# Kernel optimization log

Measured on AMD Instinct MI355X. Metric: run time of the kernel, lower is better.

## Reference

```python
import jax, jax.numpy as jnp
import numpy as np

N_NODES = 100000


def sage_conv(x, src, dst, Wl, Wr, b):
    # mean-aggregate neighbor (source) features onto destinations
    msg = x[src]                                              # [E, F]
    agg = jax.ops.segment_sum(msg, dst, num_segments=N_NODES)  # [N, F]
    deg = jax.ops.segment_sum(jnp.ones(dst.shape, x.dtype), dst, num_segments=N_NODES)
    agg = agg / jnp.maximum(deg, 1.0)[:, None]
    # PyG SAGEConv: lin_l(aggr) + lin_r(x); bias only on lin_l
    return agg @ Wl.T + x @ Wr.T + b


def setup_inputs() -> dict:
    key = jax.random.key(0)
    ks = jax.random.split(key, 12)
    d, h, c = 128, 128, 6
    s = 1.0 / np.sqrt(d)
    return {
        "x": jax.random.normal(ks[0], (N_NODES, d), jnp.float32),
        "edge_index": jax.random.randint(ks[1], (2, 3200000), 0, N_NODES, jnp.int64),
        "Wl1": jax.random.normal(ks[2], (h, d), jnp.float32) * s,
        "Wr1": jax.random.normal(ks[3], (h, d), jnp.float32) * s,
        "b1": jax.random.normal(ks[4], (h,), jnp.float32) * s,
        "Wl2": jax.random.normal(ks[5], (h, h), jnp.float32) * s,
        "Wr2": jax.random.normal(ks[6], (h, h), jnp.float32) * s,
        "b2": jax.random.normal(ks[7], (h,), jnp.float32) * s,
        "Wl3": jax.random.normal(ks[8], (c, h), jnp.float32) * s,
        "Wr3": jax.random.normal(ks[9], (c, h), jnp.float32) * s,
        "b3": jax.random.normal(ks[10], (c,), jnp.float32) * s,
    }


def reference(x, edge_index, Wl1, Wr1, b1, Wl2, Wr2, b2, Wl3, Wr3, b3):
    src, dst = edge_index[0], edge_index[1]
    h = jax.nn.relu(sage_conv(x, src, dst, Wl1, Wr1, b1))  # dropout = identity (eval)
    h = jax.nn.relu(sage_conv(h, src, dst, Wl2, Wr2, b2))
    return sage_conv(h, src, dst, Wl3, Wr3, b3)  # [N, 6]
```

## Files before the change

kernel.cpp:

```cpp
#include <hip/hip_runtime.h>
#include <hip/hip_bf16.h>

#define N_NODES 100000
#define G_PART 16
#define B_PART 96
#define NPG_PAD 6272
#define A_BLOCKS 1024

__global__ __launch_bounds__(256) void partition_edges(
    const int* __restrict__ src, const int* __restrict__ dst, int E,
    int* __restrict__ bkt, unsigned int* __restrict__ gcur, int cap, int npg) {
    __shared__ int cnt16[G_PART];
    __shared__ unsigned int base16[G_PART];
    __shared__ unsigned int cur16[G_PART];
    int tid = threadIdx.x;
    if (tid < G_PART) cnt16[tid] = 0;
    __syncthreads();
    int per = (E + A_BLOCKS - 1) / A_BLOCKS;
    int beg = blockIdx.x * per;
    int end = min(beg + per, E);
    for (int i = beg + tid; i < end; i += 256) {
        int d = dst[i];
        atomicAdd(&cnt16[d / npg], 1);
    }
    __syncthreads();
    if (tid < G_PART) {
        base16[tid] = atomicAdd(&gcur[tid], (unsigned int)cnt16[tid]);
        cur16[tid] = 0;
    }
    __syncthreads();
    for (int i = beg + tid; i < end; i += 256) {
        int d = dst[i];
        int s = src[i];
        int g = d / npg;
        unsigned int p = base16[g] + atomicAdd(&cur16[g], 1u);
        bkt[(size_t)g * cap + p] = ((d - g * npg) << 17) | s;
    }
}

__global__ __launch_bounds__(256) void count_hist(const int* __restrict__ bkt,
                                                  const unsigned int* __restrict__ gcur,
                                                  int cap, unsigned short* __restrict__ partial,
                                                  int npg, int N) {
    __shared__ int hist[NPG_PAD];
    int g = blockIdx.x & (G_PART - 1);
    int b = blockIdx.x / G_PART;
    int tid = threadIdx.x;
    for (int i = tid; i < npg; i += 256) hist[i] = 0;
    __syncthreads();
    int len = (int)gcur[g];
    int per = (len + B_PART - 1) / B_PART;
    int ibeg = b * per;
    int iend = min(ibeg + per, len);
    const int* bp = bkt + (size_t)g * cap;
    for (int i = ibeg + tid; i < iend; i += 256) {
        int v = __builtin_nontemporal_load(bp + i);
        atomicAdd(&hist[v >> 17], 1);
    }
    __syncthreads();
    size_t base = (size_t)(g * B_PART + b) * npg;
    for (int j = tid; j < npg; j += 256) partial[base + j] = (unsigned short)hist[j];
}

__global__ __launch_bounds__(256) void scan_partials(unsigned short* __restrict__ partial,
                                                     int* __restrict__ cnt,
                                                     int npg, int N) {
    int n = blockIdx.x * 256 + threadIdx.x;
    if (n >= N) return;
    int g = n / npg;
    int i = n - g * npg;
    size_t base = (size_t)g * B_PART * npg + i;
    int run = 0;
#pragma unroll 4
    for (int b = 0; b < B_PART; ++b) {
        size_t idx = base + (size_t)b * npg;
        int t = partial[idx];
        partial[idx] = (unsigned short)run;
        run += t;
    }
    cnt[n] = run;
}

__global__ __launch_bounds__(256) void fill_hist(const int* __restrict__ bkt,
                                                 const unsigned int* __restrict__ gcur,
                                                 int cap,
                                                 const unsigned short* __restrict__ partial,
                                                 const int* __restrict__ row_off,
                                                 int* __restrict__ csr_src,
                                                 int npg, int N) {
    __shared__ int cur[NPG_PAD];
    int g = blockIdx.x & (G_PART - 1);
    int b = blockIdx.x / G_PART;
    int lo = g * npg;
    int tid = threadIdx.x;
    size_t pbase = (size_t)(g * B_PART + b) * npg;
    for (int i = tid; i < npg && lo + i < N; i += 256)
        cur[i] = row_off[lo + i] + (int)partial[pbase + i];
    __syncthreads();
    int len = (int)gcur[g];
    int per = (len + B_PART - 1) / B_PART;
    int ibeg = b * per;
    int iend = min(ibeg + per, len);
    const int* bp = bkt + (size_t)g * cap;
    for (int i = ibeg + tid; i < iend; i += 256) {
        int v = __builtin_nontemporal_load(bp + i);
        int p = atomicAdd(&cur[v >> 17], 1);
        csr_src[p] = v & 0x1FFFF;
    }
}

#define SCHUNK 1024

__global__ __launch_bounds__(256) void scan_blocks(const int* __restrict__ cnt,
                                                   int* __restrict__ row_off,
                                                   int* __restrict__ block_sums, int n) {
    __shared__ int ts[256];
    int tid = threadIdx.x;
    int base = blockIdx.x * SCHUNK + tid * 4;
    int v[4];
    int s = 0;
#pragma unroll
    for (int j = 0; j < 4; ++j) {
        int i = base + j;
        v[j] = (i < n) ? cnt[i] : 0;
        s += v[j];
    }
    ts[tid] = s;
    __syncthreads();
    for (int off = 1; off < 256; off <<= 1) {
        int t = 0;
        if (tid >= off) t = ts[tid - off];
        __syncthreads();
        if (tid >= off) ts[tid] += t;
        __syncthreads();
    }
    int run = (tid > 0) ? ts[tid - 1] : 0;
    if (tid == 255) block_sums[blockIdx.x] = ts[255];
#pragma unroll
    for (int j = 0; j < 4; ++j) {
        int i = base + j;
        if (i < n) row_off[i] = run;
        run += v[j];
    }
}

__global__ __launch_bounds__(256) void scan_sums(int* __restrict__ block_sums, int nb,
                                                 int* __restrict__ row_off, int n) {
    __shared__ int ts[256];
    int tid = threadIdx.x;
    int v = (tid < nb) ? block_sums[tid] : 0;
    ts[tid] = v;
    __syncthreads();
    for (int off = 1; off < 256; off <<= 1) {
        int t = 0;
        if (tid >= off) t = ts[tid - off];
        __syncthreads();
        if (tid >= off) ts[tid] += t;
        __syncthreads();
    }
    if (tid < nb) block_sums[tid] = (tid > 0) ? ts[tid - 1] : 0;
    if (tid == 255) row_off[n] = ts[255];
}

__global__ __launch_bounds__(256) void scan_add(int* __restrict__ row_off,
                                                const int* __restrict__ block_sums, int n) {
    int tid = threadIdx.x;
    int off = block_sums[blockIdx.x];
    int base = blockIdx.x * SCHUNK + tid * 4;
#pragma unroll
    for (int j = 0; j < 4; ++j) {
        int i = base + j;
        if (i < n) row_off[i] += off;
    }
}

__global__ __launch_bounds__(256) void pack_bf16(const float* __restrict__ in,
                                                 uint2* __restrict__ out, int n4) {
    int i = blockIdx.x * 256 + threadIdx.x;
    if (i >= n4) return;
    float4 v = *(const float4*)&in[(size_t)i * 4];
    __hip_bfloat162 p0 = __float22bfloat162_rn(make_float2(v.x, v.y));
    __hip_bfloat162 p1 = __float22bfloat162_rn(make_float2(v.z, v.w));
    uint2 o;
    o.x = *(const uint*)&p0;
    o.y = *(const uint*)&p1;
    out[i] = o;
}

static __device__ inline unsigned short f2bf(float v) {
    __hip_bfloat16 b = __float2bfloat16(v);
    return *(const unsigned short*)&b;
}

__global__ __launch_bounds__(256) void pack_weights(
    const float* __restrict__ Wl1, const float* __restrict__ Wr1,
    const float* __restrict__ Wl2, const float* __restrict__ Wr2,
    const float* __restrict__ Wl3, const float* __restrict__ Wr3,
    unsigned short* __restrict__ Wc1, unsigned short* __restrict__ Wc2,
    unsigned short* __restrict__ W3c) {
    int idx = blockIdx.x * 256 + threadIdx.x;
    if (idx < 32768) {
        int n = idx >> 8, k = idx & 255;
        Wc1[idx] = f2bf((k < 128) ? Wl1[n * 128 + k] : Wr1[n * 128 + (k - 128)]);
    } else if (idx < 65536) {
        int t = idx - 32768;
        int n = t >> 8, k = t & 255;
        Wc2[t] = f2bf((k < 128) ? Wl2[n * 128 + k] : Wr2[n * 128 + (k - 128)]);
    } else if (idx < 65536 + 2048) {
        int t = idx - 65536;
        int n = t >> 7, k = t & 127;
        float v = (n < 6) ? Wl3[n * 128 + k] : ((n < 12) ? Wr3[(n - 6) * 128 + k] : 0.f);
        W3c[t] = f2bf(v);
    }
}

typedef __attribute__((ext_vector_type(8))) short bfrag8;
typedef __attribute__((ext_vector_type(4))) float f32x4;

static __device__ inline float2 unpack2(uint v) {
    float2 r;
    r.x = __uint_as_float(v << 16);
    r.y = __uint_as_float(v & 0xffff0000u);
    return r;
}

__global__ __launch_bounds__(256) void agg_gemm(
    const uint* __restrict__ featb,
    const unsigned short* __restrict__ Aself,
    const int* __restrict__ row_off,
    const int* __restrict__ csr,
    const unsigned short* __restrict__ Wc,
    const float* __restrict__ bias,
    unsigned short* __restrict__ outb,
    int do_lin3,
    const unsigned short* __restrict__ W3c,
    const float* __restrict__ b3,
    unsigned short* __restrict__ zg,
    float* __restrict__ zs,
    int M, int relu) {
    __shared__ unsigned short aggT[16][136];
    __shared__ unsigned short h2T[16][136];
    int tid = threadIdx.x;
    int wave = tid >> 6;
    int lane = tid & 63;
    int tile = blockIdx.x * 16;
    int mrow = lane & 15;
    int quad = lane >> 4;
    int row = tile + mrow;
    int rc = (row < M) ? row : 0;

    bfrag8 aself[4];
    const unsigned short* arow1 = Aself + (size_t)rc * 128;
#pragma unroll
    for (int ks = 0; ks < 4; ++ks)
        aself[ks] = *(const bfrag8*)(arow1 + ks * 32 + quad * 8);
    int t0 = wave * 2, t1 = wave * 2 + 1;
    float bc0 = bias[t0 * 16 + mrow];
    float bc1 = bias[t1 * 16 + mrow];

    for (int sub = 0; sub < 4; ++sub) {
        int node = tile + wave * 4 + sub;
        float sx = 0.f, sy = 0.f;
        float inv = 0.f;
        if (node < M) {
            int beg = row_off[node], end = row_off[node + 1];
            int i = beg;
            for (; i + 4 <= end; i += 4) {
                int s0 = csr[i], s1 = csr[i + 1], s2 = csr[i + 2], s3 = csr[i + 3];
                uint v0 = featb[(size_t)s0 * 64 + lane];
                uint v1 = featb[(size_t)s1 * 64 + lane];
                uint v2 = featb[(size_t)s2 * 64 + lane];
                uint v3 = featb[(size_t)s3 * 64 + lane];
                float2 f0 = unpack2(v0), f1 = unpack2(v1);
                float2 f2 = unpack2(v2), f3 = unpack2(v3);
                sx += f0.x + f1.x + f2.x + f3.x;
                sy += f0.y + f1.y + f2.y + f3.y;
            }
            for (; i < end; ++i) {
                uint v = featb[(size_t)csr[i] * 64 + lane];
                float2 f = unpack2(v);
                sx += f.x;
                sy += f.y;
            }
            inv = (end > beg) ? 1.0f / (float)(end - beg) : 0.0f;
        }
        __hip_bfloat162 p = __float22bfloat162_rn(make_float2(sx * inv, sy * inv));
        *(uint*)&aggT[wave * 4 + sub][lane * 2] = *(const uint*)&p;
    }
    __syncthreads();

    f32x4 acc0 = (f32x4){0.f, 0.f, 0.f, 0.f};
    f32x4 acc1 = (f32x4){0.f, 0.f, 0.f, 0.f};
#pragma unroll
    for (int ks = 0; ks < 8; ++ks) {
        bfrag8 af;
        if (ks < 4) af = *(const bfrag8*)&aggT[mrow][ks * 32 + quad * 8];
        else af = aself[ks - 4];
        bfrag8 bf0 = *(const bfrag8*)(Wc + (size_t)(t0 * 16 + mrow) * 256 + ks * 32 + quad * 8);
        bfrag8 bf1 = *(const bfrag8*)(Wc + (size_t)(t1 * 16 + mrow) * 256 + ks * 32 + quad * 8);
        acc0 = __builtin_amdgcn_mfma_f32_16x16x32_bf16(af, bf0, acc0, 0, 0, 0);
        acc1 = __builtin_amdgcn_mfma_f32_16x16x32_bf16(af, bf1, acc1, 0, 0, 0);
    }
#pragma unroll
    for (int tt = 0; tt < 2; ++tt) {
        f32x4 a = tt ? acc1 : acc0;
        int col = (wave * 2 + tt) * 16 + mrow;
        float bc = tt ? bc1 : bc0;
#pragma unroll
        for (int r = 0; r < 4; ++r) {
            float v = a[r] + bc;
            if (relu) v = fmaxf(v, 0.f);
            h2T[quad * 4 + r][col] = f2bf(v);
        }
    }
    __syncthreads();
    if (outb) {
        int r = tid >> 4;
        int c8 = (tid & 15) * 8;
        int orow = tile + r;
        if (orow < M)
            *(uint4*)&outb[(size_t)orow * 128 + c8] = *(const uint4*)&h2T[r][c8];
    }
    if (do_lin3 && wave == 0) {
        f32x4 acc = (f32x4){0.f, 0.f, 0.f, 0.f};
#pragma unroll
        for (int ks = 0; ks < 4; ++ks) {
            bfrag8 af = *(const bfrag8*)&h2T[mrow][ks * 32 + quad * 8];
            bfrag8 bf = *(const bfrag8*)(W3c + (size_t)mrow * 128 + ks * 32 + quad * 8);
            acc = __builtin_amdgcn_mfma_f32_16x16x32_bf16(af, bf, acc, 0, 0, 0);
        }
        int col = mrow;
#pragma unroll
        for (int r = 0; r < 4; ++r) {
            int orow = tile + quad * 4 + r;
            if (orow < M) {
                float v = acc[r];
                if (col < 6) {
                    zg[(size_t)orow * 8 + col] = f2bf(v);
                } else if (col < 12) {
                    zs[(size_t)orow * 6 + (col - 6)] = v + b3[col - 6];
                }
            }
        }
    }
}

__global__ void out_kernel(const unsigned short* __restrict__ zg,
                           const float* __restrict__ zs,
                           const int* __restrict__ row_off,
                           const int* __restrict__ csr,
                           float* __restrict__ out, int M) {
    int idx = blockIdx.x * blockDim.x + threadIdx.x;
    int node = idx >> 3;
    int j = idx & 7;
    if (node >= M || j >= 6) return;
    int beg = row_off[node], end = row_off[node + 1];
    float acc = 0.f;
    int i = beg;
    for (; i + 4 <= end; i += 4) {
        int s0 = csr[i], s1 = csr[i + 1], s2 = csr[i + 2], s3 = csr[i + 3];
        uint z0 = zg[(size_t)s0 * 8 + j];
        uint z1 = zg[(size_t)s1 * 8 + j];
        uint z2 = zg[(size_t)s2 * 8 + j];
        uint z3 = zg[(size_t)s3 * 8 + j];
        acc += __uint_as_float(z0 << 16) + __uint_as_float(z1 << 16) +
               __uint_as_float(z2 << 16) + __uint_as_float(z3 << 16);
    }
    for (; i < end; ++i) {
        uint z = zg[(size_t)csr[i] * 8 + j];
        acc += __uint_as_float(z << 16);
    }
    float inv = (end > beg) ? 1.0f / (float)(end - beg) : 0.0f;
    out[(size_t)node * 6 + j] = acc * inv + zs[(size_t)node * 6 + j];
}

static inline size_t align_up(size_t x, size_t a) { return (x + a - 1) & ~(a - 1); }

extern "C" void kernel_launch(void* const* d_in, const int* in_sizes, int n_in,
                              void* d_out, int out_size, void* d_ws, size_t ws_size,
                              hipStream_t stream) {
    const float* x = (const float*)d_in[0];
    const int* ei = (const int*)d_in[1];
    const float* Wl1 = (const float*)d_in[2];
    const float* Wr1 = (const float*)d_in[3];
    const float* b1 = (const float*)d_in[4];
    const float* Wl2 = (const float*)d_in[5];
    const float* Wr2 = (const float*)d_in[6];
    const float* b2 = (const float*)d_in[7];
    const float* Wl3 = (const float*)d_in[8];
    const float* Wr3 = (const float*)d_in[9];
    const float* b3 = (const float*)d_in[10];

    const int N = in_sizes[0] / 128;
    const int E = in_sizes[1] / 2;
    const int* src = ei;
    const int* dst = ei + E;

    char* ws = (char*)d_ws;
    size_t off = 0;
    int* cnt = (int*)(ws + off);        off = align_up(off + (size_t)N * 4, 512);
    int* row_off = (int*)(ws + off);    off = align_up(off + (size_t)(N + 1) * 4, 512);
    int* block_sums = (int*)(ws + off); off = align_up(off + 512 * 4, 512);
    unsigned int* gcur = (unsigned int*)(ws + off); off = align_up(off + 64 * 4, 512);
    unsigned short* Wc1 = (unsigned short*)(ws + off); off = align_up(off + 128 * 256 * 2, 512);
    unsigned short* Wc2 = (unsigned short*)(ws + off); off = align_up(off + 128 * 256 * 2, 512);
    unsigned short* W3c = (unsigned short*)(ws + off); off = align_up(off + 16 * 128 * 2, 512);
    int* csr_src = (int*)(ws + off);    off = align_up(off + (size_t)E * 4, 512);
    float* slotA = (float*)(ws + off);  off = align_up(off + (size_t)N * 128 * 4, 512);
    float* slotB = (float*)(ws + off);  off = align_up(off + (size_t)N * 128 * 4, 512);
    uint2* h1b = (uint2*)(ws + off);    off = align_up(off + (size_t)N * 128 * 2, 512);
    unsigned short* partial = (unsigned short*)slotA;
    const int cap = 210000;
    int* bkt = (int*)slotB;
    uint2* xb = (uint2*)slotA;
    unsigned short* zg = (unsigned short*)slotB;
    float* zs = (float*)((char*)slotB + align_up((size_t)N * 8 * 2, 512));
    (void)ws_size;

    const int npg = (N + G_PART - 1) / G_PART;
    const int build_grid = G_PART * B_PART;

    hipMemsetAsync(gcur, 0, G_PART * 4, stream);
    partition_edges<<<A_BLOCKS, 256, 0, stream>>>(src, dst, E, bkt, gcur, cap, npg);
    count_hist<<<build_grid, 256, 0, stream>>>(bkt, gcur, cap, partial, npg, N);
    scan_partials<<<(N + 255) / 256, 256, 0, stream>>>(partial, cnt, npg, N);

    const int nscan = (N + SCHUNK - 1) / SCHUNK;
    scan_blocks<<<nscan, 256, 0, stream>>>(cnt, row_off, block_sums, N);
    scan_sums<<<1, 256, 0, stream>>>(block_sums, nscan, row_off, N);
    scan_add<<<nscan, 256, 0, stream>>>(row_off, block_sums, N);

    fill_hist<<<build_grid, 256, 0, stream>>>(bkt, gcur, cap, partial, row_off,
                                              csr_src, npg, N);

    const int n4 = N * 32;
    pack_bf16<<<(n4 + 255) / 256, 256, 0, stream>>>(x, xb, n4);
    pack_weights<<<(65536 + 2048 + 255) / 256, 256, 0, stream>>>(
        Wl1, Wr1, Wl2, Wr2, Wl3, Wr3, Wc1, Wc2, W3c);

    int fusedGrid = (N + 15) / 16;

    agg_gemm<<<fusedGrid, 256, 0, stream>>>(
        (const uint*)xb, (const unsigned short*)xb, row_off, csr_src, Wc1, b1,
        (unsigned short*)h1b, 0, nullptr, nullptr, nullptr, nullptr, N, 1);
    agg_gemm<<<fusedGrid, 256, 0, stream>>>(
        (const uint*)h1b, (const unsigned short*)h1b, row_off, csr_src, Wc2, b2,
        nullptr, 1, W3c, b3, zg, zs, N, 1);
    out_kernel<<<(N * 8 + 255) / 256, 256, 0, stream>>>(zg, zs, row_off, csr_src,
                                                        (float*)d_out, N);
}
```

Before: 577.3 us.

## Bin CSR edges by source range and sweep source ranges across node blocks

The CSR build now sorts each destination's edges into 8 source-range sub-bins, using 128 destination partitions with finer partial histograms. The aggregation kernel handles 64 nodes per block and loops over source ranges in the outer loop, so concurrent gathers touch a narrower slice of the feature table and get better cache locality. The cost is an 8x larger offset array and scan, more per-node offset loads, 32 accumulator registers per thread with an occupancy hint, and per-tile syncs inside the GEMM loop.

```diff
diff --git a/kernel.cpp b/kernel.cpp
--- a/kernel.cpp
+++ b/kernel.cpp
@@ -2,51 +2,57 @@
 #include <hip/hip_bf16.h>
 
 #define N_NODES 100000
-#define G_PART 16
-#define B_PART 96
-#define NPG_PAD 6272
+#define G_PART 128
+#define NPG 782
+#define NR 8
+#define RNG 12500
+#define BINS (NPG * NR)
+#define BINS_PAD 6272
+#define B_PART 12
 #define A_BLOCKS 1024
+#define NBINS (N_NODES * NR)
+#define NPB 64
 
 __global__ __launch_bounds__(256) void partition_edges(
     const int* __restrict__ src, const int* __restrict__ dst, int E,
-    int* __restrict__ bkt, unsigned int* __restrict__ gcur, int cap, int npg) {
-    __shared__ int cnt16[G_PART];
-    __shared__ unsigned int base16[G_PART];
-    __shared__ unsigned int cur16[G_PART];
-    int tid = threadIdx.x;
-    if (tid < G_PART) cnt16[tid] = 0;
+    int* __restrict__ bkt, unsigned int* __restrict__ gcur, int cap) {
+    __shared__ int cnt[G_PART];
+    __shared__ unsigned int base[G_PART];
+    __shared__ unsigned int cur[G_PART];
+    int tid = threadIdx.x;
+    if (tid < G_PART) cnt[tid] = 0;
     __syncthreads();
     int per = (E + A_BLOCKS - 1) / A_BLOCKS;
     int beg = blockIdx.x * per;
     int end = min(beg + per, E);
     for (int i = beg + tid; i < end; i += 256) {
         int d = dst[i];
-        atomicAdd(&cnt16[d / npg], 1);
+        atomicAdd(&cnt[d / NPG], 1);
     }
     __syncthreads();
     if (tid < G_PART) {
-        base16[tid] = atomicAdd(&gcur[tid], (unsigned int)cnt16[tid]);
-        cur16[tid] = 0;
+        base[tid] = atomicAdd(&gcur[tid], (unsigned int)cnt[tid]);
+        cur[tid] = 0;
     }
     __syncthreads();
     for (int i = beg + tid; i < end; i += 256) {
         int d = dst[i];
         int s = src[i];
-        int g = d / npg;
-        unsigned int p = base16[g] + atomicAdd(&cur16[g], 1u);
-        bkt[(size_t)g * cap + p] = ((d - g * npg) << 17) | s;
+        int g = d / NPG;
+        unsigned int p = base[g] + atomicAdd(&cur[g], 1u);
+        bkt[(size_t)g * cap + p] = ((d - g * NPG) << 17) | s;
     }
 }
 
 __global__ __launch_bounds__(256) void count_hist(const int* __restrict__ bkt,
                                                   const unsigned int* __restrict__ gcur,
-                                                  int cap, unsigned short* __restrict__ partial,
-                                                  int npg, int N) {
-    __shared__ int hist[NPG_PAD];
+                                                  int cap,
+                                                  unsigned short* __restrict__ partial) {
+    __shared__ int hist[BINS_PAD];
     int g = blockIdx.x & (G_PART - 1);
     int b = blockIdx.x / G_PART;
     int tid = threadIdx.x;
-    for (int i = tid; i < npg; i += 256) hist[i] = 0;
+    for (int i = tid; i < BINS; i += 256) hist[i] = 0;
     __syncthreads();
     int len = (int)gcur[g];
     int per = (len + B_PART - 1) / B_PART;
@@ -55,47 +61,113 @@
     const int* bp = bkt + (size_t)g * cap;
     for (int i = ibeg + tid; i < iend; i += 256) {
         int v = __builtin_nontemporal_load(bp + i);
-        atomicAdd(&hist[v >> 17], 1);
-    }
-    __syncthreads();
-    size_t base = (size_t)(g * B_PART + b) * npg;
-    for (int j = tid; j < npg; j += 256) partial[base + j] = (unsigned short)hist[j];
+        int bin = (v >> 17) * NR + (v & 0x1FFFF) / RNG;
+        atomicAdd(&hist[bin], 1);
+    }
+    __syncthreads();
+    size_t basep = (size_t)(g * B_PART + b) * BINS;
+    for (int j = tid; j < BINS; j += 256) partial[basep + j] = (unsigned short)hist[j];
 }
 
 __global__ __launch_bounds__(256) void scan_partials(unsigned short* __restrict__ partial,
-                                                     int* __restrict__ cnt,
-                                                     int npg, int N) {
-    int n = blockIdx.x * 256 + threadIdx.x;
-    if (n >= N) return;
-    int g = n / npg;
-    int i = n - g * npg;
-    size_t base = (size_t)g * B_PART * npg + i;
+                                                     int* __restrict__ cnt) {
+    int B = blockIdx.x * 256 + threadIdx.x;
+    if (B >= NBINS) return;
+    int g = B / BINS;
+    int i = B - g * BINS;
+    size_t basep = (size_t)g * B_PART * BINS + i;
     int run = 0;
 #pragma unroll 4
     for (int b = 0; b < B_PART; ++b) {
-        size_t idx = base + (size_t)b * npg;
+        size_t idx = basep + (size_t)b * BINS;
         int t = partial[idx];
         partial[idx] = (unsigned short)run;
         run += t;
     }
-    cnt[n] = run;
+    cnt[B] = run;
+}
+
+#define SCHUNK 4096
+
+__global__ __launch_bounds__(256) void scan_blocks(const int* __restrict__ cnt,
+                                                   int* __restrict__ boff,
+                                                   int* __restrict__ block_sums, int n) {
+    __shared__ int ts[256];
+    int tid = threadIdx.x;
+    int base = blockIdx.x * SCHUNK + tid * 16;
+    int v[16];
+    int s = 0;
+#pragma unroll
+    for (int j = 0; j < 16; ++j) {
+        int i = base + j;
+        v[j] = (i < n) ? cnt[i] : 0;
+        s += v[j];
+    }
+    ts[tid] = s;
+    __syncthreads();
+    for (int off = 1; off < 256; off <<= 1) {
+        int t = 0;
+        if (tid >= off) t = ts[tid - off];
+        __syncthreads();
+        if (tid >= off) ts[tid] += t;
+        __syncthreads();
+    }
+    int run = (tid > 0) ? ts[tid - 1] : 0;
+    if (tid == 255) block_sums[blockIdx.x] = ts[255];
+#pragma unroll
+    for (int j = 0; j < 16; ++j) {
+        int i = base + j;
+        if (i < n) boff[i] = run;
+        run += v[j];
+    }
+}
+
+__global__ __launch_bounds__(256) void scan_sums(int* __restrict__ block_sums, int nb,
+                                                 int* __restrict__ boff, int n) {
+    __shared__ int ts[256];
+    int tid = threadIdx.x;
+    int v = (tid < nb) ? block_sums[tid] : 0;
+    ts[tid] = v;
+    __syncthreads();
+    for (int off = 1; off < 256; off <<= 1) {
+        int t = 0;
+        if (tid >= off) t = ts[tid - off];
+        __syncthreads();
+        if (tid >= off) ts[tid] += t;
+        __syncthreads();
+    }
+    if (tid < nb) block_sums[tid] = (tid > 0) ? ts[tid - 1] : 0;
+    if (tid == 255) boff[n] = ts[255];
+}
+
+__global__ __launch_bounds__(256) void scan_add(int* __restrict__ boff,
+                                                const int* __restrict__ block_sums, int n) {
+    int tid = threadIdx.x;
+    int off = block_sums[blockIdx.x];
+    int base = blockIdx.x * SCHUNK + tid * 16;
+#pragma unroll
+    for (int j = 0; j < 16; ++j) {
+        int i = base + j;
+        if (i < n) boff[i] += off;
+    }
 }
 
 __global__ __launch_bounds__(256) void fill_hist(const int* __restrict__ bkt,
                                                  const unsigned int* __restrict__ gcur,
                                                  int cap,
                                                  const unsigned short* __restrict__ partial,
-                                                 const int* __restrict__ row_off,
-                                                 int* __restrict__ csr_src,
-                                                 int npg, int N) {
-    __shared__ int cur[NPG_PAD];
+                                                 const int* __restrict__ boff,
+                                                 int* __restrict__ csr_src) {
+    __shared__ int cur[BINS_PAD];
     int g = blockIdx.x & (G_PART - 1);
     int b = blockIdx.x / G_PART;
-    int lo = g * npg;
-    int tid = threadIdx.x;
-    size_t pbase = (size_t)(g * B_PART + b) * npg;
-    for (int i = tid; i < npg && lo + i < N; i += 256)
-        cur[i] = row_off[lo + i] + (int)partial[pbase + i];
+    int tid = threadIdx.x;
+    size_t pbase = (size_t)(g * B_PART + b) * BINS;
+    int gb = g * BINS;
+    for (int i = tid; i < BINS; i += 256) {
+        int node = g * NPG + (i >> 3);
+        if (node < N_NODES) cur[i] = boff[gb + i] + (int)partial[pbase + i];
+    }
     __syncthreads();
     int len = (int)gcur[g];
     int per = (len + B_PART - 1) / B_PART;
@@ -104,73 +176,9 @@
     const int* bp = bkt + (size_t)g * cap;
     for (int i = ibeg + tid; i < iend; i += 256) {
         int v = __builtin_nontemporal_load(bp + i);
-        int p = atomicAdd(&cur[v >> 17], 1);
+        int bin = (v >> 17) * NR + (v & 0x1FFFF) / RNG;
+        int p = atomicAdd(&cur[bin], 1);
         csr_src[p] = v & 0x1FFFF;
-    }
-}
-
-#define SCHUNK 1024
-
-__global__ __launch_bounds__(256) void scan_blocks(const int* __restrict__ cnt,
-                                                   int* __restrict__ row_off,
-                                                   int* __restrict__ block_sums, int n) {
-    __shared__ int ts[256];
-    int tid = threadIdx.x;
-    int base = blockIdx.x * SCHUNK + tid * 4;
-    int v[4];
-    int s = 0;
-#pragma unroll
-    for (int j = 0; j < 4; ++j) {
-        int i = base + j;
-        v[j] = (i < n) ? cnt[i] : 0;
-        s += v[j];
-    }
-    ts[tid] = s;
-    __syncthreads();
-    for (int off = 1; off < 256; off <<= 1) {
-        int t = 0;
-        if (tid >= off) t = ts[tid - off];
-        __syncthreads();
-        if (tid >= off) ts[tid] += t;
-        __syncthreads();
-    }
-    int run = (tid > 0) ? ts[tid - 1] : 0;
-    if (tid == 255) block_sums[blockIdx.x] = ts[255];
-#pragma unroll
-    for (int j = 0; j < 4; ++j) {
-        int i = base + j;
-        if (i < n) row_off[i] = run;
-        run += v[j];
-    }
-}
-
-__global__ __launch_bounds__(256) void scan_sums(int* __restrict__ block_sums, int nb,
-                                                 int* __restrict__ row_off, int n) {
-    __shared__ int ts[256];
-    int tid = threadIdx.x;
-    int v = (tid < nb) ? block_sums[tid] : 0;
-    ts[tid] = v;
-    __syncthreads();
-    for (int off = 1; off < 256; off <<= 1) {
-        int t = 0;
-        if (tid >= off) t = ts[tid - off];
-        __syncthreads();
-        if (tid >= off) ts[tid] += t;
-        __syncthreads();
-    }
-    if (tid < nb) block_sums[tid] = (tid > 0) ? ts[tid - 1] : 0;
-    if (tid == 255) row_off[n] = ts[255];
-}
-
-__global__ __launch_bounds__(256) void scan_add(int* __restrict__ row_off,
-                                                const int* __restrict__ block_sums, int n) {
-    int tid = threadIdx.x;
-    int off = block_sums[blockIdx.x];
-    int base = blockIdx.x * SCHUNK + tid * 4;
-#pragma unroll
-    for (int j = 0; j < 4; ++j) {
-        int i = base + j;
-        if (i < n) row_off[i] += off;
     }
 }
 
@@ -224,10 +232,10 @@
     return r;
 }
 
-__global__ __launch_bounds__(256) void agg_gemm(
+__global__ __launch_bounds__(256, 6) void agg_gemm(
     const uint* __restrict__ featb,
     const unsigned short* __restrict__ Aself,
-    const int* __restrict__ row_off,
+    const int* __restrict__ boff,
     const int* __restrict__ csr,
     const unsigned short* __restrict__ Wc,
     const float* __restrict__ bias,
@@ -243,118 +251,141 @@
     int tid = threadIdx.x;
     int wave = tid >> 6;
     int lane = tid & 63;
-    int tile = blockIdx.x * 16;
     int mrow = lane & 15;
     int quad = lane >> 4;
-    int row = tile + mrow;
-    int rc = (row < M) ? row : 0;
-
-    bfrag8 aself[4];
-    const unsigned short* arow1 = Aself + (size_t)rc * 128;
-#pragma unroll
-    for (int ks = 0; ks < 4; ++ks)
-        aself[ks] = *(const bfrag8*)(arow1 + ks * 32 + quad * 8);
+    int base = blockIdx.x * NPB;
+
+    float accx[16], accy[16];
+#pragma unroll
+    for (int k = 0; k < 16; ++k) { accx[k] = 0.f; accy[k] = 0.f; }
+
+    for (int r = 0; r < NR; ++r) {
+#pragma unroll
+        for (int k = 0; k < 16; ++k) {
+            int node = base + (k >> 2) * 16 + wave * 4 + (k & 3);
+            if (node < M) {
+                const int* bo = boff + node * NR + r;
+                int beg = bo[0], end = bo[1];
+                float sx = accx[k], sy = accy[k];
+                int i = beg;
+                for (; i + 4 <= end; i += 4) {
+                    int s0 = csr[i], s1 = csr[i + 1], s2 = csr[i + 2], s3 = csr[i + 3];
+                    uint v0 = featb[(size_t)s0 * 64 + lane];
+                    uint v1 = featb[(size_t)s1 * 64 + lane];
+                    uint v2 = featb[(size_t)s2 * 64 + lane];
+                    uint v3 = featb[(size_t)s3 * 64 + lane];
+                    float2 f0 = unpack2(v0), f1 = unpack2(v1);
+                    float2 f2 = unpack2(v2), f3 = unpack2(v3);
+                    sx += f0.x + f1.x + f2.x + f3.x;
+                    sy += f0.y + f1.y + f2.y + f3.y;
+                }
+                for (; i < end; ++i) {
+                    uint v = featb[(size_t)csr[i] * 64 + lane];
+                    float2 f = unpack2(v);
+                    sx += f.x;
+                    sy += f.y;
+                }
+                accx[k] = sx;
+                accy[k] = sy;
+            }
+        }
+    }
+
     int t0 = wave * 2, t1 = wave * 2 + 1;
     float bc0 = bias[t0 * 16 + mrow];
     float bc1 = bias[t1 * 16 + mrow];
 
-    for (int sub = 0; sub < 4; ++sub) {
-        int node = tile + wave * 4 + sub;
-        float sx = 0.f, sy = 0.f;
-        float inv = 0.f;
-        if (node < M) {
-            int beg = row_off[node], end = row_off[node + 1];
-            int i = beg;
-            for (; i + 4 <= end; i += 4) {
-                int s0 = csr[i], s1 = csr[i + 1], s2 = csr[i + 2], s3 = csr[i + 3];
-                uint v0 = featb[(size_t)s0 * 64 + lane];
-                uint v1 = featb[(size_t)s1 * 64 + lane];
-                uint v2 = featb[(size_t)s2 * 64 + lane];
-                uint v3 = featb[(size_t)s3 * 64 + lane];
-                float2 f0 = unpack2(v0), f1 = unpack2(v1);
-                float2 f2 = unpack2(v2), f3 = unpack2(v3);
-                sx += f0.x + f1.x + f2.x + f3.x;
-                sy += f0.y + f1.y + f2.y + f3.y;
+#pragma unroll
+    for (int t = 0; t < 4; ++t) {
+        int tile = base + t * 16;
+#pragma unroll
+        for (int sub = 0; sub < 4; ++sub) {
+            int node = tile + wave * 4 + sub;
+            float inv = 0.f;
+            if (node < M) {
+                int b0 = boff[node * NR], e0 = boff[node * NR + NR];
+                inv = (e0 > b0) ? 1.0f / (float)(e0 - b0) : 0.f;
             }
-            for (; i < end; ++i) {
-                uint v = featb[(size_t)csr[i] * 64 + lane];
-                float2 f = unpack2(v);
-                sx += f.x;
-                sy += f.y;
+            __hip_bfloat162 p = __float22bfloat162_rn(
+                make_float2(accx[t * 4 + sub] * inv, accy[t * 4 + sub] * inv));
+            *(uint*)&aggT[wave * 4 + sub][lane * 2] = *(const uint*)&p;
+        }
+        int row = tile + mrow;
+        int rc = (row < M) ? row : 0;
+        const unsigned short* arow = Aself + (size_t)rc * 128;
+        bfrag8 aself[4];
+#pragma unroll
+        for (int ks = 0; ks < 4; ++ks)
+            aself[ks] = *(const bfrag8*)(arow + ks * 32 + quad * 8);
+        __syncthreads();
+        f32x4 acc0 = (f32x4){0.f, 0.f, 0.f, 0.f};
+        f32x4 acc1 = (f32x4){0.f, 0.f, 0.f, 0.f};
+#pragma unroll
+        for (int ks = 0; ks < 8; ++ks) {
+            bfrag8 af;
+            if (ks < 4) af = *(const bfrag8*)&aggT[mrow][ks * 32 + quad * 8];
+            else af = aself[ks - 4];
+            bfrag8 bf0 = *(const bfrag8*)(Wc + (size_t)(t0 * 16 + mrow) * 256 + ks * 32 + quad * 8);
+            bfrag8 bf1 = *(const bfrag8*)(Wc + (size_t)(t1 * 16 + mrow) * 256 + ks * 32 + quad * 8);
+            acc0 = __builtin_amdgcn_mfma_f32_16x16x32_bf16(af, bf0, acc0, 0, 0, 0);
+            acc1 = __builtin_amdgcn_mfma_f32_16x16x32_bf16(af, bf1, acc1, 0, 0, 0);
+        }
+#pragma unroll
+        for (int tt = 0; tt < 2; ++tt) {
+            f32x4 a = tt ? acc1 : acc0;
+            int col = (wave * 2 + tt) * 16 + mrow;
+            float bc = tt ? bc1 : bc0;
+#pragma unroll
+            for (int rr = 0; rr < 4; ++rr) {
+                float v = a[rr] + bc;
+                if (relu) v = fmaxf(v, 0.f);
+                h2T[quad * 4 + rr][col] = f2bf(v);
             }
-            inv = (end > beg) ? 1.0f / (float)(end - beg) : 0.0f;
-        }
-        __hip_bfloat162 p = __float22bfloat162_rn(make_float2(sx * inv, sy * inv));
-        *(uint*)&aggT[wave * 4 + sub][lane * 2] = *(const uint*)&p;
-    }
-    __syncthreads();
-
-    f32x4 acc0 = (f32x4){0.f, 0.f, 0.f, 0.f};
-    f32x4 acc1 = (f32x4){0.f, 0.f, 0.f, 0.f};
-#pragma unroll
-    for (int ks = 0; ks < 8; ++ks) {
-        bfrag8 af;
-        if (ks < 4) af = *(const bfrag8*)&aggT[mrow][ks * 32 + quad * 8];
-        else af = aself[ks - 4];
-        bfrag8 bf0 = *(const bfrag8*)(Wc + (size_t)(t0 * 16 + mrow) * 256 + ks * 32 + quad * 8);
-        bfrag8 bf1 = *(const bfrag8*)(Wc + (size_t)(t1 * 16 + mrow) * 256 + ks * 32 + quad * 8);
-        acc0 = __builtin_amdgcn_mfma_f32_16x16x32_bf16(af, bf0, acc0, 0, 0, 0);
-        acc1 = __builtin_amdgcn_mfma_f32_16x16x32_bf16(af, bf1, acc1, 0, 0, 0);
-    }
-#pragma unroll
-    for (int tt = 0; tt < 2; ++tt) {
-        f32x4 a = tt ? acc1 : acc0;
-        int col = (wave * 2 + tt) * 16 + mrow;
-        float bc = tt ? bc1 : bc0;
-#pragma unroll
-        for (int r = 0; r < 4; ++r) {
-            float v = a[r] + bc;
-            if (relu) v = fmaxf(v, 0.f);
-            h2T[quad * 4 + r][col] = f2bf(v);
-        }
-    }
-    __syncthreads();
-    if (outb) {
-        int r = tid >> 4;
-        int c8 = (tid & 15) * 8;
-        int orow = tile + r;
-        if (orow < M)
-            *(uint4*)&outb[(size_t)orow * 128 + c8] = *(const uint4*)&h2T[r][c8];
-    }
-    if (do_lin3 && wave == 0) {
-        f32x4 acc = (f32x4){0.f, 0.f, 0.f, 0.f};
-#pragma unroll
-        for (int ks = 0; ks < 4; ++ks) {
-            bfrag8 af = *(const bfrag8*)&h2T[mrow][ks * 32 + quad * 8];
-            bfrag8 bf = *(const bfrag8*)(W3c + (size_t)mrow * 128 + ks * 32 + quad * 8);
-            acc = __builtin_amdgcn_mfma_f32_16x16x32_bf16(af, bf, acc, 0, 0, 0);
-        }
-        int col = mrow;
-#pragma unroll
-        for (int r = 0; r < 4; ++r) {
-            int orow = tile + quad * 4 + r;
-            if (orow < M) {
-                float v = acc[r];
-                if (col < 6) {
-                    zg[(size_t)orow * 8 + col] = f2bf(v);
-                } else if (col < 12) {
-                    zs[(size_t)orow * 6 + (col - 6)] = v + b3[col - 6];
+        }
+        __syncthreads();
+        if (outb) {
+            int rr = tid >> 4;
+            int c8 = (tid & 15) * 8;
+            int orow = tile + rr;
+            if (orow < M)
+                *(uint4*)&outb[(size_t)orow * 128 + c8] = *(const uint4*)&h2T[rr][c8];
+        }
+        if (do_lin3 && wave == 0) {
+            f32x4 acc = (f32x4){0.f, 0.f, 0.f, 0.f};
+#pragma unroll
+            for (int ks = 0; ks < 4; ++ks) {
+                bfrag8 af = *(const bfrag8*)&h2T[mrow][ks * 32 + quad * 8];
+                bfrag8 bf = *(const bfrag8*)(W3c + (size_t)mrow * 128 + ks * 32 + quad * 8);
+                acc = __builtin_amdgcn_mfma_f32_16x16x32_bf16(af, bf, acc, 0, 0, 0);
+            }
+            int col = mrow;
+#pragma unroll
+            for (int rr = 0; rr < 4; ++rr) {
+                int orow = tile + quad * 4 + rr;
+                if (orow < M) {
+                    float v = acc[rr];
+                    if (col < 6) {
+                        zg[(size_t)orow * 8 + col] = f2bf(v);
+                    } else if (col < 12) {
+                        zs[(size_t)orow * 6 + (col - 6)] = v + b3[col - 6];
+                    }
                 }
             }
         }
+        __syncthreads();
     }
 }
 
 __global__ void out_kernel(const unsigned short* __restrict__ zg,
                            const float* __restrict__ zs,
-                           const int* __restrict__ row_off,
+                           const int* __restrict__ boff,
                            const int* __restrict__ csr,
                            float* __restrict__ out, int M) {
     int idx = blockIdx.x * blockDim.x + threadIdx.x;
     int node = idx >> 3;
     int j = idx & 7;
     if (node >= M || j >= 6) return;
-    int beg = row_off[node], end = row_off[node + 1];
+    int beg = boff[node * NR], end = boff[node * NR + NR];
     float acc = 0.f;
     int i = beg;
     for (; i + 4 <= end; i += 4) {
@@ -398,10 +429,10 @@
 
     char* ws = (char*)d_ws;
     size_t off = 0;
-    int* cnt = (int*)(ws + off);        off = align_up(off + (size_t)N * 4, 512);
-    int* row_off = (int*)(ws + off);    off = align_up(off + (size_t)(N + 1) * 4, 512);
+    int* cnt = (int*)(ws + off);        off = align_up(off + (size_t)NBINS * 4, 512);
+    int* boff = (int*)(ws + off);       off = align_up(off + (size_t)(NBINS + 1) * 4, 512);
     int* block_sums = (int*)(ws + off); off = align_up(off + 512 * 4, 512);
-    unsigned int* gcur = (unsigned int*)(ws + off); off = align_up(off + 64 * 4, 512);
+    unsigned int* gcur = (unsigned int*)(ws + off); off = align_up(off + G_PART * 4, 512);
     unsigned short* Wc1 = (unsigned short*)(ws + off); off = align_up(off + 128 * 256 * 2, 512);
     unsigned short* Wc2 = (unsigned short*)(ws + off); off = align_up(off + 128 * 256 * 2, 512);
     unsigned short* W3c = (unsigned short*)(ws + off); off = align_up(off + 16 * 128 * 2, 512);
@@ -410,42 +441,40 @@
     float* slotB = (float*)(ws + off);  off = align_up(off + (size_t)N * 128 * 4, 512);
     uint2* h1b = (uint2*)(ws + off);    off = align_up(off + (size_t)N * 128 * 2, 512);
     unsigned short* partial = (unsigned short*)slotA;
-    const int cap = 210000;
+    const int cap = 28000;
     int* bkt = (int*)slotB;
     uint2* xb = (uint2*)slotA;
     unsigned short* zg = (unsigned short*)slotB;
     float* zs = (float*)((char*)slotB + align_up((size_t)N * 8 * 2, 512));
     (void)ws_size;
 
-    const int npg = (N + G_PART - 1) / G_PART;
     const int build_grid = G_PART * B_PART;
 
     hipMemsetAsync(gcur, 0, G_PART * 4, stream);
-    partition_edges<<<A_BLOCKS, 256, 0, stream>>>(src, dst, E, bkt, gcur, cap, npg);
-    count_hist<<<build_grid, 256, 0, stream>>>(bkt, gcur, cap, partial, npg, N);
-    scan_partials<<<(N + 255) / 256, 256, 0, stream>>>(partial, cnt, npg, N);
-
-    const int nscan = (N + SCHUNK - 1) / SCHUNK;
-    scan_blocks<<<nscan, 256, 0, stream>>>(cnt, row_off, block_sums, N);
-    scan_sums<<<1, 256, 0, stream>>>(block_sums, nscan, row_off, N);
-    scan_add<<<nscan, 256, 0, stream>>>(row_off, block_sums, N);
-
-    fill_hist<<<build_grid, 256, 0, stream>>>(bkt, gcur, cap, partial, row_off,
-                                              csr_src, npg, N);
+    partition_edges<<<A_BLOCKS, 256, 0, stream>>>(src, dst, E, bkt, gcur, cap);
+    count_hist<<<build_grid, 256, 0, stream>>>(bkt, gcur, cap, partial);
+    scan_partials<<<(NBINS + 255) / 256, 256, 0, stream>>>(partial, cnt);
+
+    const int nscan = (NBINS + SCHUNK - 1) / SCHUNK;
+    scan_blocks<<<nscan, 256, 0, stream>>>(cnt, boff, block_sums, NBINS);
+    scan_sums<<<1, 256, 0, stream>>>(block_sums, nscan, boff, NBINS);
+    scan_add<<<nscan, 256, 0, stream>>>(boff, block_sums, NBINS);
+
+    fill_hist<<<build_grid, 256, 0, stream>>>(bkt, gcur, cap, partial, boff, csr_src);
 
     const int n4 = N * 32;
     pack_bf16<<<(n4 + 255) / 256, 256, 0, stream>>>(x, xb, n4);
     pack_weights<<<(65536 + 2048 + 255) / 256, 256, 0, stream>>>(
         Wl1, Wr1, Wl2, Wr2, Wl3, Wr3, Wc1, Wc2, W3c);
 
-    int fusedGrid = (N + 15) / 16;
-
-    agg_gemm<<<fusedGrid, 256, 0, stream>>>(
-        (const uint*)xb, (const unsigned short*)xb, row_off, csr_src, Wc1, b1,
+    const int aggGrid = (N + NPB - 1) / NPB;
+
+    agg_gemm<<<aggGrid, 256, 0, stream>>>(
+        (const uint*)xb, (const unsigned short*)xb, boff, csr_src, Wc1, b1,
         (unsigned short*)h1b, 0, nullptr, nullptr, nullptr, nullptr, N, 1);
-    agg_gemm<<<fusedGrid, 256, 0, stream>>>(
-        (const uint*)h1b, (const unsigned short*)h1b, row_off, csr_src, Wc2, b2,
+    agg_gemm<<<aggGrid, 256, 0, stream>>>(
+        (const uint*)h1b, (const unsigned short*)h1b, boff, csr_src, Wc2, b2,
         nullptr, 1, W3c, b3, zg, zs, N, 1);
-    out_kernel<<<(N * 8 + 255) / 256, 256, 0, stream>>>(zg, zs, row_off, csr_src,
+    out_kernel<<<(N * 8 + 255) / 256, 256, 0, stream>>>(zg, zs, boff, csr_src,
                                                         (float*)d_out, N);
 }
```

Measured after the change: 1.568 ms. 2.72x slower.
